# Kernel tuning notes

Hardware: AMD Instinct MI355X
Metric: run time of the kernel (lower is better)

The kernel has to match this reference:

```python
import jax, jax.numpy as jnp
import numpy as np

B, K, L = 256, 32, 4096
SIGMA = 1.5
EPS = 1e-5
PEAK_LAMBDA = 0.005
ORTHO_LAMBDA = 20000.0


def setup_inputs() -> dict:
    key = jax.random.key(0)
    a = jax.random.uniform(key, (1, B, K, L), dtype=jnp.float32)
    # attention maps are distributions over the L (clip/time) axis
    a = a / a.sum(-1, keepdims=True)
    return {"attns": a}


def reference(attns):
    a = attns[-1]  # [B, K, L]
    b, k, l = a.shape

    # --- peak loss: Gaussian target centered at argmax index (constant wrt a) ---
    idx = jnp.argmax(a, axis=2)  # [B, K] int
    x = jnp.arange(l, dtype=a.dtype)  # [L]
    diff = (x[None, None, :] - idx[..., None].astype(a.dtype)) / SIGMA
    g = jnp.exp(-0.5 * diff * diff)  # [B, K, L]
    g = g / g.sum(-1, keepdims=True)

    p = a + EPS
    t = g + EPS
    # F.kl_div(p.log(), t, reduction='sum') = sum(t * (log t - log p))
    peak_loss = PEAK_LAMBDA * jnp.sum(t * (jnp.log(t) - jnp.log(p)))

    # --- ortho loss on the epsilon-shifted attns (in-place += eps in torch) ---
    dot = jnp.einsum('bkl,bml->bkm', p, p)  # [B, K, K]
    eye = jnp.eye(k, dtype=a.dtype)
    mask = 1.0 - eye  # zero out diagonal
    ortho_loss = ORTHO_LAMBDA * jnp.mean((dot * mask - eye * mask) ** 2)

    loss = peak_loss + ortho_loss
    return (loss, peak_loss, ortho_loss)
```

## Files before the change

kernel.cpp:

```cpp
#include <hip/hip_runtime.h>
#include <hip/hip_bf16.h>

#define NB 256
#define NK 32
#define NL 4096
#define NC 8
#define CH 512
#define EPSV 1e-5f
#define PEAK_LAMBDA 0.005f
#define ORTHO_LAMBDA 20000.0f
#define LN2F 0.6931471805599453f

typedef __attribute__((ext_vector_type(8))) short short8;
typedef __attribute__((ext_vector_type(4))) float f32x4;

__global__ __launch_bounds__(256) void k_main(const float* __restrict__ a,
                                              float* __restrict__ gram,
                                              float* __restrict__ rmax,
                                              int* __restrict__ ridx,
                                              float* __restrict__ rlogp) {
    const int bc = blockIdx.x;
    const int b = bc >> 3, chk = bc & 7;
    const int tid = threadIdx.x;
    const int lane = tid & 63, wv = tid >> 6;
    const int r0 = lane & 15, hi = lane >> 4;

    const float* __restrict__ rowA =
        a + ((size_t)b * NK + r0) * NL + chk * CH + wv * 128 + hi * 8;
    const float* __restrict__ rowB = rowA + 16 * (size_t)NL;
    const int lbase = chk * CH + wv * 128 + hi * 8;

    float mvA = -1.0f, mvB = -1.0f;
    int miA = 0, miB = 0;
    float lpA0 = 0.0f, lpA1 = 0.0f, lpB0 = 0.0f, lpB1 = 0.0f;
    f32x4 acc00 = {0.f,0.f,0.f,0.f}, acc01 = {0.f,0.f,0.f,0.f},
          acc11 = {0.f,0.f,0.f,0.f};

#pragma unroll
    for (int s = 0; s < 4; ++s) {
        float4 a0 = *reinterpret_cast<const float4*>(rowA + s * 32);
        float4 a1 = *reinterpret_cast<const float4*>(rowA + s * 32 + 4);
        float4 b0 = *reinterpret_cast<const float4*>(rowB + s * 32);
        float4 b1 = *reinterpret_cast<const float4*>(rowB + s * 32 + 4);
        float va[8] = {a0.x, a0.y, a0.z, a0.w, a1.x, a1.y, a1.z, a1.w};
        float vb[8] = {b0.x, b0.y, b0.z, b0.w, b1.x, b1.y, b1.z, b1.w};
        const int l0 = lbase + s * 32;
        union { unsigned u[4]; short8 s8; } fa, fb;
#pragma unroll
        for (int c2 = 0; c2 < 4; ++c2) {
            float v0 = va[2*c2], v1 = va[2*c2 + 1];
            float w0 = vb[2*c2], w1 = vb[2*c2 + 1];
            float xa0 = v0 + EPSV, xa1 = v1 + EPSV;
            float xb0 = w0 + EPSV, xb1 = w1 + EPSV;
            if (v0 > mvA) { mvA = v0; miA = l0 + 2*c2; }
            if (v1 > mvA) { mvA = v1; miA = l0 + 2*c2 + 1; }
            if (w0 > mvB) { mvB = w0; miB = l0 + 2*c2; }
            if (w1 > mvB) { mvB = w1; miB = l0 + 2*c2 + 1; }
            lpA0 += __log2f(xa0); lpA1 += __log2f(xa1);
            lpB0 += __log2f(xb0); lpB1 += __log2f(xb1);
            fa.u[c2] = __builtin_amdgcn_perm(__float_as_uint(xa1),
                                             __float_as_uint(xa0), 0x07060302u);
            fb.u[c2] = __builtin_amdgcn_perm(__float_as_uint(xb1),
                                             __float_as_uint(xb0), 0x07060302u);
        }
        acc00 = __builtin_amdgcn_mfma_f32_16x16x32_bf16(fa.s8, fa.s8, acc00, 0, 0, 0);
        acc01 = __builtin_amdgcn_mfma_f32_16x16x32_bf16(fa.s8, fb.s8, acc01, 0, 0, 0);
        acc11 = __builtin_amdgcn_mfma_f32_16x16x32_bf16(fb.s8, fb.s8, acc11, 0, 0, 0);
    }
    float lpA = (lpA0 + lpA1) * LN2F;
    float lpB = (lpB0 + lpB1) * LN2F;

#pragma unroll
    for (int off = 16; off <= 32; off <<= 1) {
        float ov = __shfl_xor(mvA, off); int oi = __shfl_xor(miA, off);
        if (ov > mvA || (ov == mvA && oi < miA)) { mvA = ov; miA = oi; }
        ov = __shfl_xor(mvB, off); oi = __shfl_xor(miB, off);
        if (ov > mvB || (ov == mvB && oi < miB)) { mvB = ov; miB = oi; }
        lpA += __shfl_xor(lpA, off);
        lpB += __shfl_xor(lpB, off);
    }

    __shared__ float s_mv[4][32], s_lp[4][32];
    __shared__ int   s_mi[4][32];
    __shared__ float gbuf[4][768];

    if (hi == 0) {
        s_mv[wv][r0] = mvA; s_mi[wv][r0] = miA; s_lp[wv][r0] = lpA;
        s_mv[wv][16 + r0] = mvB; s_mi[wv][16 + r0] = miB; s_lp[wv][16 + r0] = lpB;
    }
    {
        const int rb2 = hi * 4;
#pragma unroll
        for (int r = 0; r < 4; ++r) {
            int gr = rb2 + r;
            gbuf[wv][gr * 16 + r0]       = acc00[r];
            gbuf[wv][256 + gr * 16 + r0] = acc01[r];
            gbuf[wv][512 + gr * 16 + r0] = acc11[r];
        }
    }
    __syncthreads();

    if (tid < 32) {
        float bv = -1.0f, lp = 0.0f; int bi = 0;
#pragma unroll
        for (int w = 0; w < 4; ++w) {
            float v = s_mv[w][tid]; int i = s_mi[w][tid];
            if (v > bv || (v == bv && i < bi)) { bv = v; bi = i; }
            lp += s_lp[w][tid];
        }
        rmax[bc * 32 + tid] = bv;
        ridx[bc * 32 + tid] = bi;
        rlogp[bc * 32 + tid] = lp;
    }
#pragma unroll
    for (int j = 0; j < 3; ++j) {
        int e = tid + 256 * j;
        gram[(size_t)bc * 768 + e] =
            gbuf[0][e] + gbuf[1][e] + gbuf[2][e] + gbuf[3][e];
    }
}

__global__ __launch_bounds__(256) void k_fin(const float* __restrict__ a,
                                             const float* __restrict__ gram,
                                             const float* __restrict__ rmax,
                                             const int* __restrict__ ridx,
                                             const float* __restrict__ rlogp,
                                             float* __restrict__ bpeak,
                                             float* __restrict__ bortho) {
    const int b = blockIdx.x;
    const int tid = threadIdx.x;
    __shared__ int idx_s[32];
    __shared__ float lp_s[32];
    __shared__ float rkl_s[32];
    __shared__ float red[256];

    float local = 0.0f;
#pragma unroll
    for (int j = 0; j < 3; ++j) {
        int e = tid + 256 * j;
        float s = 0.0f;
#pragma unroll
        for (int ch = 0; ch < NC; ++ch)
            s += gram[(size_t)(b * NC + ch) * 768 + e];
        int blk = e >> 8, idx = e & 255, k = idx >> 4, m = idx & 15;
        float w = (blk == 1) ? 2.0f : ((k == m) ? 0.0f : 1.0f);
        local += w * s * s;
    }

    if (tid < 32) {
        float bv = -1.0f; int bi = 0; float lp = 0.0f;
#pragma unroll
        for (int ch = 0; ch < NC; ++ch) {
            float v = rmax[(b * NC + ch) * 32 + tid];
            int i = ridx[(b * NC + ch) * 32 + tid];
            if (v > bv || (v == bv && i < bi)) { bv = v; bi = i; }
            lp += rlogp[(b * NC + ch) * 32 + tid];
        }
        idx_s[tid] = bi; lp_s[tid] = lp;
    }
    __syncthreads();

    const int r = tid >> 3, cc = tid & 7;
    const int idx = idx_s[r];
    const float* __restrict__ arow = a + ((size_t)b * 32 + r) * (size_t)NL;
    float gv[8], pvv[8];
    float zs = 0.0f;
#pragma unroll
    for (int w = 0; w < 8; ++w) {
        int l = idx - 31 + cc + 8 * w;
        float d = (float)(cc + 8 * w - 31);
        float g = __expf(d * d * (-1.0f / 4.5f));
        if (l >= 0 && l < NL) { gv[w] = g; zs += g; pvv[w] = arow[l]; }
        else { gv[w] = 0.0f; pvv[w] = 1.0f; }
    }
    zs += __shfl_xor(zs, 1); zs += __shfl_xor(zs, 2); zs += __shfl_xor(zs, 4);
    const float rz = 1.0f / zs;
    float tlt = 0.0f, tlp = 0.0f;
#pragma unroll
    for (int w = 0; w < 8; ++w) {
        int l = idx - 31 + cc + 8 * w;
        if (l >= 0 && l < NL) {
            float gg = gv[w] * rz;
            float tf = gg + EPSV;
            tlt += tf * __logf(tf);
            tlp += gg * __logf(pvv[w] + EPSV);
        }
    }
    tlt += __shfl_xor(tlt, 1); tlt += __shfl_xor(tlt, 2); tlt += __shfl_xor(tlt, 4);
    tlp += __shfl_xor(tlp, 1); tlp += __shfl_xor(tlp, 2); tlp += __shfl_xor(tlp, 4);
    if (cc == 0) {
        int lo = max(0, idx - 31), hi2 = min(NL - 1, idx + 32);
        int nv = hi2 - lo + 1;
        rkl_s[r] = tlt + (float)(NL - nv) * EPSV * __logf(EPSV)
                 - tlp - EPSV * lp_s[r];
    }
    red[tid] = local;
    __syncthreads();
    for (int s = 128; s > 0; s >>= 1) {
        if (tid < s) red[tid] += red[tid + s];
        __syncthreads();
    }
    if (tid == 0) bortho[b] = red[0];
    __syncthreads();
    red[tid] = (tid < 32) ? rkl_s[tid] : 0.0f;
    __syncthreads();
    for (int s = 128; s > 0; s >>= 1) {
        if (tid < s) red[tid] += red[tid + s];
        __syncthreads();
    }
    if (tid == 0) bpeak[b] = red[0];
}

__global__ __launch_bounds__(256) void k_final(const float* __restrict__ bpeak,
                                               const float* __restrict__ bortho,
                                               float* __restrict__ out) {
    const int tid = threadIdx.x;
    __shared__ float s1[256], s2[256];
    s1[tid] = bpeak[tid];
    s2[tid] = bortho[tid];
    __syncthreads();
    for (int s = 128; s > 0; s >>= 1) {
        if (tid < s) { s1[tid] += s1[tid + s]; s2[tid] += s2[tid + s]; }
        __syncthreads();
    }
    if (tid == 0) {
        float peak = PEAK_LAMBDA * s1[0];
        float ortho = ORTHO_LAMBDA * (s2[0] / (float)(NB * NK * NK));
        out[0] = peak + ortho;
        out[1] = peak;
        out[2] = ortho;
    }
}

extern "C" void kernel_launch(void* const* d_in, const int* in_sizes, int n_in,
                              void* d_out, int out_size, void* d_ws, size_t ws_size,
                              hipStream_t stream) {
    const float* a = (const float*)d_in[0];
    float* out = (float*)d_out;
    float* ws = (float*)d_ws;
    float* gram  = ws;
    float* rmax  = gram + (size_t)NB * NC * 768;
    int*   ridxp = (int*)(rmax + NB * NC * 32);
    float* rlogp = (float*)(ridxp + NB * NC * 32);
    float* bpeak = rlogp + NB * NC * 32;
    float* bortho = bpeak + NB;

    k_main<<<NB * NC, 256, 0, stream>>>(a, gram, rmax, ridxp, rlogp);
    k_fin<<<NB, 256, 0, stream>>>(a, gram, rmax, ridxp, rlogp, bpeak, bortho);
    k_final<<<1, 256, 0, stream>>>(bpeak, bortho, out);
}
```

Baseline: 40.11 us.

## Split finalize kernel into per-row wave blocks and separate ortho partial blocks

Replaces the per-batch 256-thread finalize kernel with a 64-thread-per-block kernel: 8192 blocks each handle one (b,k) row's argmax merge and Gaussian-window KL using wave shuffles, and 512 extra blocks reduce the gram partials. The final kernel now sums 8192 row values and 512 ortho partials. The aim is more parallelism and no block-level barrier reductions in the middle stage, at the cost of many tiny blocks and a larger final reduction.

```diff
diff --git a/kernel.cpp b/kernel.cpp
--- a/kernel.cpp
+++ b/kernel.cpp
@@ -120,104 +120,91 @@
     }
 }
 
-__global__ __launch_bounds__(256) void k_fin(const float* __restrict__ a,
+__global__ __launch_bounds__(64) void k_fin2(const float* __restrict__ a,
                                              const float* __restrict__ gram,
                                              const float* __restrict__ rmax,
                                              const int* __restrict__ ridx,
                                              const float* __restrict__ rlogp,
-                                             float* __restrict__ bpeak,
-                                             float* __restrict__ bortho) {
-    const int b = blockIdx.x;
-    const int tid = threadIdx.x;
-    __shared__ int idx_s[32];
-    __shared__ float lp_s[32];
-    __shared__ float rkl_s[32];
-    __shared__ float red[256];
-
-    float local = 0.0f;
-#pragma unroll
-    for (int j = 0; j < 3; ++j) {
-        int e = tid + 256 * j;
-        float s = 0.0f;
-#pragma unroll
-        for (int ch = 0; ch < NC; ++ch)
-            s += gram[(size_t)(b * NC + ch) * 768 + e];
-        int blk = e >> 8, idx = e & 255, k = idx >> 4, m = idx & 15;
-        float w = (blk == 1) ? 2.0f : ((k == m) ? 0.0f : 1.0f);
-        local += w * s * s;
-    }
-
-    if (tid < 32) {
-        float bv = -1.0f; int bi = 0; float lp = 0.0f;
-#pragma unroll
-        for (int ch = 0; ch < NC; ++ch) {
-            float v = rmax[(b * NC + ch) * 32 + tid];
-            int i = ridx[(b * NC + ch) * 32 + tid];
-            if (v > bv || (v == bv && i < bi)) { bv = v; bi = i; }
-            lp += rlogp[(b * NC + ch) * 32 + tid];
-        }
-        idx_s[tid] = bi; lp_s[tid] = lp;
-    }
-    __syncthreads();
-
-    const int r = tid >> 3, cc = tid & 7;
-    const int idx = idx_s[r];
-    const float* __restrict__ arow = a + ((size_t)b * 32 + r) * (size_t)NL;
-    float gv[8], pvv[8];
-    float zs = 0.0f;
-#pragma unroll
-    for (int w = 0; w < 8; ++w) {
-        int l = idx - 31 + cc + 8 * w;
-        float d = (float)(cc + 8 * w - 31);
-        float g = __expf(d * d * (-1.0f / 4.5f));
-        if (l >= 0 && l < NL) { gv[w] = g; zs += g; pvv[w] = arow[l]; }
-        else { gv[w] = 0.0f; pvv[w] = 1.0f; }
-    }
-    zs += __shfl_xor(zs, 1); zs += __shfl_xor(zs, 2); zs += __shfl_xor(zs, 4);
-    const float rz = 1.0f / zs;
-    float tlt = 0.0f, tlp = 0.0f;
-#pragma unroll
-    for (int w = 0; w < 8; ++w) {
-        int l = idx - 31 + cc + 8 * w;
-        if (l >= 0 && l < NL) {
-            float gg = gv[w] * rz;
+                                             float* __restrict__ rowkl,
+                                             float* __restrict__ ortho_parts) {
+    const int bid = blockIdx.x;
+    const int lane = threadIdx.x;
+
+    if (bid < NB * NK) {
+        const int b = bid >> 5, k = bid & 31;
+        float bv = -1.0f, lp = 0.0f; int bi = 0;
+        if (lane < NC) {
+            bv = rmax[(b * NC + lane) * 32 + k];
+            bi = ridx[(b * NC + lane) * 32 + k];
+            lp = rlogp[(b * NC + lane) * 32 + k];
+        }
+#pragma unroll
+        for (int off = 1; off <= 4; off <<= 1) {
+            float ov = __shfl_xor(bv, off); int oi = __shfl_xor(bi, off);
+            float ol = __shfl_xor(lp, off);
+            if (ov > bv || (ov == bv && oi < bi)) { bv = ov; bi = oi; }
+            lp += ol;
+        }
+        const int idx = __shfl(bi, 0);
+        const float lpr = __shfl(lp, 0);
+
+        const int l = idx - 31 + lane;
+        const float d = (float)(lane - 31);
+        const bool valid = (l >= 0) && (l < NL);
+        const float g = valid ? __expf(d * d * (-1.0f / 4.5f)) : 0.0f;
+        const float pv = valid
+            ? a[((size_t)b * NK + k) * (size_t)NL + l] : 1.0f;
+        float zs = g;
+#pragma unroll
+        for (int off = 1; off < 64; off <<= 1) zs += __shfl_xor(zs, off);
+        const float rz = 1.0f / zs;
+        float term = 0.0f;
+        int nv = valid ? 1 : 0;
+        if (valid) {
+            float gg = g * rz;
             float tf = gg + EPSV;
-            tlt += tf * __logf(tf);
-            tlp += gg * __logf(pvv[w] + EPSV);
-        }
-    }
-    tlt += __shfl_xor(tlt, 1); tlt += __shfl_xor(tlt, 2); tlt += __shfl_xor(tlt, 4);
-    tlp += __shfl_xor(tlp, 1); tlp += __shfl_xor(tlp, 2); tlp += __shfl_xor(tlp, 4);
-    if (cc == 0) {
-        int lo = max(0, idx - 31), hi2 = min(NL - 1, idx + 32);
-        int nv = hi2 - lo + 1;
-        rkl_s[r] = tlt + (float)(NL - nv) * EPSV * __logf(EPSV)
-                 - tlp - EPSV * lp_s[r];
-    }
-    red[tid] = local;
-    __syncthreads();
-    for (int s = 128; s > 0; s >>= 1) {
-        if (tid < s) red[tid] += red[tid + s];
-        __syncthreads();
-    }
-    if (tid == 0) bortho[b] = red[0];
-    __syncthreads();
-    red[tid] = (tid < 32) ? rkl_s[tid] : 0.0f;
-    __syncthreads();
-    for (int s = 128; s > 0; s >>= 1) {
-        if (tid < s) red[tid] += red[tid + s];
-        __syncthreads();
-    }
-    if (tid == 0) bpeak[b] = red[0];
-}
-
-__global__ __launch_bounds__(256) void k_final(const float* __restrict__ bpeak,
-                                               const float* __restrict__ bortho,
+            term = tf * __logf(tf) - gg * __logf(pv + EPSV);
+        }
+#pragma unroll
+        for (int off = 1; off < 64; off <<= 1) {
+            term += __shfl_xor(term, off);
+            nv += __shfl_xor(nv, off);
+        }
+        if (lane == 0)
+            rowkl[bid] = term + (float)(NL - nv) * (EPSV * __logf(EPSV))
+                       - EPSV * lpr;
+    } else {
+        const int gid = bid - NB * NK;
+        float local = 0.0f;
+#pragma unroll
+        for (int j = 0; j < 6; ++j) {
+            int eg = gid * 384 + j * 64 + lane;
+            int b = eg / 768, e = eg - b * 768;
+            float s = 0.0f;
+#pragma unroll
+            for (int ch = 0; ch < NC; ++ch)
+                s += gram[(size_t)(b * NC + ch) * 768 + e];
+            int blk = e >> 8, idx2 = e & 255, kk = idx2 >> 4, mm = idx2 & 15;
+            float w = (blk == 1) ? 2.0f : ((kk == mm) ? 0.0f : 1.0f);
+            local += w * s * s;
+        }
+#pragma unroll
+        for (int off = 1; off < 64; off <<= 1) local += __shfl_xor(local, off);
+        if (lane == 0) ortho_parts[gid] = local;
+    }
+}
+
+__global__ __launch_bounds__(256) void k_final(const float* __restrict__ rowkl,
+                                               const float* __restrict__ ortho_parts,
                                                float* __restrict__ out) {
     const int tid = threadIdx.x;
     __shared__ float s1[256], s2[256];
-    s1[tid] = bpeak[tid];
-    s2[tid] = bortho[tid];
+    float pk = 0.0f, ot = 0.0f;
+#pragma unroll
+    for (int j = 0; j < 32; ++j) pk += rowkl[tid + 256 * j];
+    ot = ortho_parts[tid] + ortho_parts[tid + 256];
+    s1[tid] = pk;
+    s2[tid] = ot;
     __syncthreads();
     for (int s = 128; s > 0; s >>= 1) {
         if (tid < s) { s1[tid] += s1[tid + s]; s2[tid] += s2[tid + s]; }
@@ -242,10 +229,11 @@
     float* rmax  = gram + (size_t)NB * NC * 768;
     int*   ridxp = (int*)(rmax + NB * NC * 32);
     float* rlogp = (float*)(ridxp + NB * NC * 32);
-    float* bpeak = rlogp + NB * NC * 32;
-    float* bortho = bpeak + NB;
+    float* rowkl = rlogp + NB * NC * 32;
+    float* ortho_parts = rowkl + NB * NK;
 
     k_main<<<NB * NC, 256, 0, stream>>>(a, gram, rmax, ridxp, rlogp);
-    k_fin<<<NB, 256, 0, stream>>>(a, gram, rmax, ridxp, rlogp, bpeak, bortho);
-    k_final<<<1, 256, 0, stream>>>(bpeak, bortho, out);
-}
+    k_fin2<<<NB * NK + 512, 64, 0, stream>>>(a, gram, rmax, ridxp, rlogp,
+                                             rowkl, ortho_parts);
+    k_final<<<1, 256, 0, stream>>>(rowkl, ortho_parts, out);
+}
```

After: 36.13 us. 1.11x faster.
